# Kernel optimization log

Hardware: AMD Instinct MI355X
Metric: run time of the kernel (lower is better)

Reference implementation:

```python
import jax, jax.numpy as jnp
import numpy as np

NUM_ITEMS = 10000
EMBED_DIM = 64
USER_PERSPECTIVE_IMPORTANCE = 0.5
LEAKY_SLOPE = 0.2
BATCH = 32
MAX_HIST = 200


def setup_inputs() -> dict:
    key = jax.random.key(0)
    k_ids, k_len, k_items, k_user, k_w, k_b = jax.random.split(key, 6)
    batch_history_ids = jax.random.randint(k_ids, (BATCH, MAX_HIST), 0, NUM_ITEMS, dtype=jnp.int32)
    # lengths must be >= 1 to avoid all-masked softmax rows
    batch_history_lengths = jnp.maximum(
        jax.random.randint(k_len, (BATCH,), 0, MAX_HIST, dtype=jnp.int32), 1)
    items_embedding = jax.random.normal(k_items, (NUM_ITEMS, EMBED_DIM), dtype=jnp.float32)
    user_embedding = jax.random.normal(k_user, (1, EMBED_DIM), dtype=jnp.float32)
    fc_weight = jax.random.normal(k_w, (EMBED_DIM, EMBED_DIM), dtype=jnp.float32) * (1.0 / np.sqrt(EMBED_DIM))
    fc_bias = jax.random.normal(k_b, (EMBED_DIM,), dtype=jnp.float32) * 0.01
    return {
        'batch_history_ids': batch_history_ids,
        'batch_history_lengths': batch_history_lengths,
        'items_embedding': items_embedding,
        'user_embedding': user_embedding,
        'fc_weight': fc_weight,
        'fc_bias': fc_bias,
    }


def reference(batch_history_ids, batch_history_lengths, items_embedding, user_embedding, fc_weight, fc_bias):
    # valid[b, n] = n < length[b]
    valid = jnp.arange(MAX_HIST)[None, :] < batch_history_lengths[:, None]  # [B, N]

    hist_emb = items_embedding[batch_history_ids]  # [B, N, F] ragged gather (padded)

    # item-perspective attention: [B, I, N]
    item_att = jnp.einsum('if,bnf->bin', items_embedding, hist_emb)
    # original adds -inf mask then leaky_relu; leaky_relu(-inf) = -inf -> softmax weight 0
    item_att = jnp.where(valid[:, None, :], jax.nn.leaky_relu(item_att, LEAKY_SLOPE), -jnp.inf)
    item_scores = jax.nn.softmax(item_att, axis=-1)  # [B, I, N]

    # user-perspective attention: constant across the item-query axis (q=1, repeated over I),
    # so compute once as [B, N] and broadcast (same math as 'qif,bnf->bqin').
    user_att = jnp.einsum('f,bnf->bn', user_embedding[0], hist_emb)
    user_att = jnp.where(valid, jax.nn.leaky_relu(user_att, LEAKY_SLOPE), -jnp.inf)
    user_scores = jax.nn.softmax(user_att, axis=-1)  # [B, N]

    w = USER_PERSPECTIVE_IMPORTANCE
    attn = (1.0 - w) * item_scores + w * user_scores[:, None, :]  # [B, I, N]

    personalized = jnp.einsum('bin,bnf->bif', attn, hist_emb)  # [B, I, F]
    projected = personalized @ fc_weight.T + fc_bias  # [B, I, F]
    # final per-item score: dot with item embedding
    return jnp.einsum('bif,if->bi', projected, items_embedding)  # [B, I]
```

## Files before the change

### kernel.cpp

```cpp
#include <hip/hip_runtime.h>
#include <hip/hip_bf16.h>
#include <math.h>

#define NUM_ITEMS 10000
#define EMBED_DIM 64
#define MAX_HIST 200
#define NPAD 208
#define BATCH 32
#define LEAKY 0.2f
#define W_USER 0.5f
#define LOG2E 1.4426950408889634f
#define ECLAMP 110.0f

typedef short bf16x8 __attribute__((ext_vector_type(8)));
typedef float f32x4 __attribute__((ext_vector_type(4)));

__device__ __forceinline__ unsigned short f2bf(float f) {
    __hip_bfloat16 h = __float2bfloat16(f);
    return __builtin_bit_cast(unsigned short, h);
}

__device__ __forceinline__ float fexp2(float x) {
#if __has_builtin(__builtin_amdgcn_exp2f)
    return __builtin_amdgcn_exp2f(x);
#else
    return exp2f(x);
#endif
}

__global__ __launch_bounds__(256) void prep_kernel(const int* __restrict__ ids,
                                                   const int* __restrict__ lens,
                                                   const float* __restrict__ items,
                                                   const float* __restrict__ user,
                                                   const float* __restrict__ W,
                                                   const float* __restrict__ bias,
                                                   unsigned short* __restrict__ items_att_bf,
                                                   unsigned short* __restrict__ wti_bf,
                                                   float* __restrict__ bdot,
                                                   unsigned short* __restrict__ hist_bf,
                                                   unsigned short* __restrict__ uh_bf) {
    const int tid = threadIdx.x;
    __shared__ float shW[EMBED_DIM * EMBED_DIM];
    __shared__ float red[8];
    __shared__ float sh_usf[NPAD];
    __shared__ float sh_uh[4][EMBED_DIM];

    if (blockIdx.x < NUM_ITEMS / 4) {
        for (int idx = tid; idx < EMBED_DIM * EMBED_DIM; idx += 256) shW[idx] = W[idx];
        __syncthreads();

        const int i = blockIdx.x * 4 + (tid >> 6);
        const int g = tid & 63;
        const float* irow = items + i * EMBED_DIM;

        float acc = 0.f;
#pragma unroll
        for (int f = 0; f < EMBED_DIM; ++f) acc += irow[f] * shW[f * EMBED_DIM + g];

        wti_bf[i * EMBED_DIM + g] = f2bf(acc);
        items_att_bf[i * EMBED_DIM + g] = f2bf(irow[g] * LOG2E);

        float bv = bias[g] * irow[g];
#pragma unroll
        for (int o = 32; o > 0; o >>= 1) bv += __shfl_xor(bv, o, 64);
        if (g == 0) bdot[i] = bv;
    } else {
        const int b = blockIdx.x - NUM_ITEMS / 4;

        for (int idx = tid; idx < NPAD * 8; idx += 256) {
            const int n = idx >> 3, q = idx & 7;
            bf16x8 v = (bf16x8)0;
            if (n < MAX_HIST) {
                const int id = ids[b * MAX_HIST + n];
                const float4* p = (const float4*)(items + id * EMBED_DIM + q * 8);
                float4 v0 = p[0], v1 = p[1];
                v[0] = (short)f2bf(v0.x); v[1] = (short)f2bf(v0.y);
                v[2] = (short)f2bf(v0.z); v[3] = (short)f2bf(v0.w);
                v[4] = (short)f2bf(v1.x); v[5] = (short)f2bf(v1.y);
                v[6] = (short)f2bf(v1.z); v[7] = (short)f2bf(v1.w);
            }
            *(bf16x8*)(hist_bf + (size_t)(b * NPAD + n) * EMBED_DIM + q * 8) = v;
        }

        const int len = lens[b];
        float s = -INFINITY;
        if (tid < len) {
            const int id = ids[b * MAX_HIST + tid];
            const float* h = items + id * EMBED_DIM;
            float a0 = 0.f, a1 = 0.f;
#pragma unroll
            for (int f = 0; f < EMBED_DIM; f += 2) {
                a0 += user[f] * h[f];
                a1 += user[f + 1] * h[f + 1];
            }
            float a = a0 + a1;
            s = fmaxf(a, LEAKY * a);
        }
        float m = s;
#pragma unroll
        for (int o = 32; o > 0; o >>= 1) m = fmaxf(m, __shfl_xor(m, o, 64));
        if ((tid & 63) == 0) red[tid >> 6] = m;
        __syncthreads();
        m = fmaxf(fmaxf(red[0], red[1]), fmaxf(red[2], red[3]));

        float e = (tid < len) ? __expf(s - m) : 0.f;
        float t = e;
#pragma unroll
        for (int o = 32; o > 0; o >>= 1) t += __shfl_xor(t, o, 64);
        if ((tid & 63) == 0) red[4 + (tid >> 6)] = t;
        __syncthreads();
        const float sum = red[4] + red[5] + red[6] + red[7];

        if (tid < NPAD) sh_usf[tid] = (tid < len) ? (e / sum) : 0.f;
        __syncthreads();

        const int f = tid & 63;
        const int part = tid >> 6;
        float uhp = 0.f;
        for (int n = part; n < len; n += 4)
            uhp += sh_usf[n] * items[(size_t)ids[b * MAX_HIST + n] * EMBED_DIM + f];
        sh_uh[part][f] = uhp;
        __syncthreads();
        if (tid < EMBED_DIM)
            uh_bf[b * EMBED_DIM + tid] =
                f2bf(sh_uh[0][tid] + sh_uh[1][tid] + sh_uh[2][tid] + sh_uh[3][tid]);
    }
}

__global__ __launch_bounds__(256) void main_kernel(const unsigned short* __restrict__ items_att_bf,
                                                   const unsigned short* __restrict__ wti_bf,
                                                   const float* __restrict__ bdot,
                                                   const unsigned short* __restrict__ hist_bf,
                                                   const unsigned short* __restrict__ uh_bf,
                                                   const int* __restrict__ lens,
                                                   float* __restrict__ out) {
    const int b = blockIdx.y;
    const int tid = threadIdx.x;
    const int lane = tid & 63;
    const int w = tid >> 6;

    __shared__ __align__(16) unsigned short sh_hist[NPAD * EMBED_DIM];

    const int len = lens[b];
    const int ntiles = (len + 15) >> 4;

    const int c16 = lane & 15;
    const int g = lane >> 4;
    const int i0 = blockIdx.x * 128 + w * 32;
    const int iA = i0 + c16;
    const int iB = i0 + 16 + c16;

    bf16x8 itfA0 = *(const bf16x8*)(items_att_bf + (size_t)iA * 64 + g * 8);
    bf16x8 itfA1 = *(const bf16x8*)(items_att_bf + (size_t)iA * 64 + 32 + g * 8);
    bf16x8 wtfA0 = *(const bf16x8*)(wti_bf + (size_t)iA * 64 + g * 8);
    bf16x8 wtfA1 = *(const bf16x8*)(wti_bf + (size_t)iA * 64 + 32 + g * 8);
    bf16x8 itfB0 = *(const bf16x8*)(items_att_bf + (size_t)iB * 64 + g * 8);
    bf16x8 itfB1 = *(const bf16x8*)(items_att_bf + (size_t)iB * 64 + 32 + g * 8);
    bf16x8 wtfB0 = *(const bf16x8*)(wti_bf + (size_t)iB * 64 + g * 8);
    bf16x8 wtfB1 = *(const bf16x8*)(wti_bf + (size_t)iB * 64 + 32 + g * 8);
    bf16x8 u0 = *(const bf16x8*)(uh_bf + b * 64 + g * 8);
    bf16x8 u1 = *(const bf16x8*)(uh_bf + b * 64 + 32 + g * 8);

    const float4* src = (const float4*)(hist_bf + (size_t)b * NPAD * EMBED_DIM);
    const int nf4 = ntiles * 16 * 8;
    for (int c = tid; c < nf4; c += 256) {
        const int n = c >> 3, q = c & 7;
        float4 v = src[c];
        const int byte = (n * 128 + q * 16) ^ ((n & 7) << 4);
        *(float4*)((char*)sh_hist + byte) = v;
    }
    __syncthreads();

    if (i0 >= NUM_ITEMS) return;

    f32x4 sufA = (f32x4)0.f, sufB = (f32x4)0.f;
    sufA = __builtin_amdgcn_mfma_f32_16x16x32_bf16(u0, wtfA0, sufA, 0, 0, 0);
    sufA = __builtin_amdgcn_mfma_f32_16x16x32_bf16(u1, wtfA1, sufA, 0, 0, 0);
    sufB = __builtin_amdgcn_mfma_f32_16x16x32_bf16(u0, wtfB0, sufB, 0, 0, 0);
    sufB = __builtin_amdgcn_mfma_f32_16x16x32_bf16(u1, wtfB1, sufB, 0, 0, 0);
    const float SuA = sufA[0];
    const float SuB = sufB[0];

    float SeA = 0.f, ShA = 0.f, SeB = 0.f, ShB = 0.f;

    const char* hbase = (const char*)sh_hist;
#define LDA(T, X0, X1)                                                   \
    {                                                                    \
        const int n_ = (T) * 16 + c16;                                   \
        const int base_ = n_ * 128, sw_ = (n_ & 7) << 4;                 \
        X0 = *(const bf16x8*)(hbase + ((base_ + g * 16) ^ sw_));         \
        X1 = *(const bf16x8*)(hbase + ((base_ + 64 + g * 16) ^ sw_));    \
    }

#define EPI(S, H, Se, Sh, MASKED, NB)                                    \
    {                                                                    \
        float s0 = fminf(fmaxf(S[0], LEAKY * S[0]), ECLAMP);             \
        float s1 = fminf(fmaxf(S[1], LEAKY * S[1]), ECLAMP);             \
        float s2 = fminf(fmaxf(S[2], LEAKY * S[2]), ECLAMP);             \
        float s3 = fminf(fmaxf(S[3], LEAKY * S[3]), ECLAMP);             \
        if (MASKED) {                                                    \
            s0 = ((NB) + 0 < len) ? s0 : -INFINITY;                      \
            s1 = ((NB) + 1 < len) ? s1 : -INFINITY;                      \
            s2 = ((NB) + 2 < len) ? s2 : -INFINITY;                      \
            s3 = ((NB) + 3 < len) ? s3 : -INFINITY;                      \
        }                                                                \
        const float e0 = fexp2(s0), e1 = fexp2(s1);                      \
        const float e2 = fexp2(s2), e3 = fexp2(s3);                      \
        Se += (e0 + e1) + (e2 + e3);                                     \
        Sh = fmaf(e0, H[0], fmaf(e1, H[1], fmaf(e2, H[2], fmaf(e3, H[3], Sh)))); \
    }

#define MFMA8(A0, A1, SA, HA, SB, HB)                                     \
    SA = __builtin_amdgcn_mfma_f32_16x16x32_bf16(A0, itfA0, SA, 0, 0, 0); \
    SA = __builtin_amdgcn_mfma_f32_16x16x32_bf16(A1, itfA1, SA, 0, 0, 0); \
    SB = __builtin_amdgcn_mfma_f32_16x16x32_bf16(A0, itfB0, SB, 0, 0, 0); \
    SB = __builtin_amdgcn_mfma_f32_16x16x32_bf16(A1, itfB1, SB, 0, 0, 0); \
    HA = __builtin_amdgcn_mfma_f32_16x16x32_bf16(A0, wtfA0, HA, 0, 0, 0); \
    HA = __builtin_amdgcn_mfma_f32_16x16x32_bf16(A1, wtfA1, HA, 0, 0, 0); \
    HB = __builtin_amdgcn_mfma_f32_16x16x32_bf16(A0, wtfB0, HB, 0, 0, 0); \
    HB = __builtin_amdgcn_mfma_f32_16x16x32_bf16(A1, wtfB1, HB, 0, 0, 0);

    bf16x8 a0, a1;
    LDA(0, a0, a1)

    for (int t = 0; t < ntiles - 1; ++t) {
        f32x4 SA = (f32x4)0.f, HA = (f32x4)0.f, SB = (f32x4)0.f, HB = (f32x4)0.f;
        MFMA8(a0, a1, SA, HA, SB, HB)
        bf16x8 p0, p1;
        LDA(t + 1, p0, p1)
        const int nb = t * 16 + g * 4;
        (void)nb;
        EPI(SA, HA, SeA, ShA, 0, 0)
        EPI(SB, HB, SeB, ShB, 0, 0)
        a0 = p0; a1 = p1;
    }
    {
        f32x4 SA = (f32x4)0.f, HA = (f32x4)0.f, SB = (f32x4)0.f, HB = (f32x4)0.f;
        MFMA8(a0, a1, SA, HA, SB, HB)
        const int nb = (ntiles - 1) * 16 + g * 4;
        EPI(SA, HA, SeA, ShA, 1, nb)
        EPI(SB, HB, SeB, ShB, 1, nb)
    }
#undef MFMA8
#undef EPI
#undef LDA

    SeA += __shfl_xor(SeA, 16, 64); SeA += __shfl_xor(SeA, 32, 64);
    ShA += __shfl_xor(ShA, 16, 64); ShA += __shfl_xor(ShA, 32, 64);
    SeB += __shfl_xor(SeB, 16, 64); SeB += __shfl_xor(SeB, 32, 64);
    ShB += __shfl_xor(ShB, 16, 64); ShB += __shfl_xor(ShB, 32, 64);

    if (g == 0) {
        if (iA < NUM_ITEMS)
            out[(size_t)b * NUM_ITEMS + iA] =
                (1.0f - W_USER) * (ShA / SeA) + W_USER * SuA + bdot[iA];
        if (iB < NUM_ITEMS)
            out[(size_t)b * NUM_ITEMS + iB] =
                (1.0f - W_USER) * (ShB / SeB) + W_USER * SuB + bdot[iB];
    }
}

extern "C" void kernel_launch(void* const* d_in, const int* in_sizes, int n_in,
                              void* d_out, int out_size, void* d_ws, size_t ws_size,
                              hipStream_t stream) {
    const int* ids = (const int*)d_in[0];
    const int* lens = (const int*)d_in[1];
    const float* items = (const float*)d_in[2];
    const float* user = (const float*)d_in[3];
    const float* W = (const float*)d_in[4];
    const float* bias = (const float*)d_in[5];
    float* out = (float*)d_out;

    char* p = (char*)d_ws;
    unsigned short* items_att_bf = (unsigned short*)p; p += (size_t)NUM_ITEMS * EMBED_DIM * 2;
    unsigned short* wti_bf       = (unsigned short*)p; p += (size_t)NUM_ITEMS * EMBED_DIM * 2;
    float* bdot                  = (float*)p;          p += (size_t)NUM_ITEMS * 4;
    unsigned short* hist_bf      = (unsigned short*)p; p += (size_t)BATCH * NPAD * EMBED_DIM * 2;
    unsigned short* uh_bf        = (unsigned short*)p; p += (size_t)BATCH * EMBED_DIM * 2;

    prep_kernel<<<NUM_ITEMS / 4 + BATCH, 256, 0, stream>>>(ids, lens, items, user, W, bias,
                                                           items_att_bf, wti_bf, bdot,
                                                           hist_bf, uh_bf);

    dim3 grid((NUM_ITEMS + 127) / 128, BATCH);
    main_kernel<<<grid, 256, 0, stream>>>(items_att_bf, wti_bf, bdot, hist_bf, uh_bf, lens, out);
}
```

Measured before the change: 47.45 us.

## Amortize history staging over more items per block and shrink prep grid

The main kernel now covers 256 items per block instead of 128. Each wave processes four 16-item groups one after another, with the next group's item fragments prefetched, so the per-block LDS staging of the history tile is amortized over more items. The prep kernel uses 157 blocks, each handling 64 items in a loop, instead of 2500 tiny blocks. The user-weighted history sum now reads the bf16 history cached in LDS instead of re-gathering from global memory. The trade-offs are half as many main-kernel blocks (fewer waves in flight) and a serial dependency across item groups within each wave.

```diff
diff --git a/kernel.cpp b/kernel.cpp
--- a/kernel.cpp
+++ b/kernel.cpp
@@ -11,6 +11,7 @@
 #define W_USER 0.5f
 #define LOG2E 1.4426950408889634f
 #define ECLAMP 110.0f
+#define NWTI 157
 
 typedef short bf16x8 __attribute__((ext_vector_type(8)));
 typedef float f32x4 __attribute__((ext_vector_type(4)));
@@ -18,6 +19,10 @@
 __device__ __forceinline__ unsigned short f2bf(float f) {
     __hip_bfloat16 h = __float2bfloat16(f);
     return __builtin_bit_cast(unsigned short, h);
+}
+
+__device__ __forceinline__ float bf2f(unsigned short u) {
+    return __builtin_bit_cast(float, (unsigned int)u << 16);
 }
 
 __device__ __forceinline__ float fexp2(float x) {
@@ -40,32 +45,40 @@
                                                    unsigned short* __restrict__ hist_bf,
                                                    unsigned short* __restrict__ uh_bf) {
     const int tid = threadIdx.x;
-    __shared__ float shW[EMBED_DIM * EMBED_DIM];
+    __shared__ __align__(16) char sbuf[NPAD * EMBED_DIM * 2];
     __shared__ float red[8];
     __shared__ float sh_usf[NPAD];
     __shared__ float sh_uh[4][EMBED_DIM];
 
-    if (blockIdx.x < NUM_ITEMS / 4) {
+    if (blockIdx.x < NWTI) {
+        float* shW = (float*)sbuf;
         for (int idx = tid; idx < EMBED_DIM * EMBED_DIM; idx += 256) shW[idx] = W[idx];
         __syncthreads();
 
-        const int i = blockIdx.x * 4 + (tid >> 6);
         const int g = tid & 63;
-        const float* irow = items + i * EMBED_DIM;
-
-        float acc = 0.f;
-#pragma unroll
-        for (int f = 0; f < EMBED_DIM; ++f) acc += irow[f] * shW[f * EMBED_DIM + g];
-
-        wti_bf[i * EMBED_DIM + g] = f2bf(acc);
-        items_att_bf[i * EMBED_DIM + g] = f2bf(irow[g] * LOG2E);
-
-        float bv = bias[g] * irow[g];
-#pragma unroll
-        for (int o = 32; o > 0; o >>= 1) bv += __shfl_xor(bv, o, 64);
-        if (g == 0) bdot[i] = bv;
+        const int isub = tid >> 6;
+        const int base = blockIdx.x * 64 + isub * 16;
+
+        for (int k = 0; k < 16; ++k) {
+            const int i = base + k;
+            if (i >= NUM_ITEMS) break;
+            const float* irow = items + (size_t)i * EMBED_DIM;
+
+            float acc = 0.f;
+#pragma unroll
+            for (int f = 0; f < EMBED_DIM; ++f) acc += irow[f] * shW[f * EMBED_DIM + g];
+
+            wti_bf[i * EMBED_DIM + g] = f2bf(acc);
+            items_att_bf[i * EMBED_DIM + g] = f2bf(irow[g] * LOG2E);
+
+            float bv = bias[g] * irow[g];
+#pragma unroll
+            for (int o = 32; o > 0; o >>= 1) bv += __shfl_xor(bv, o, 64);
+            if (g == 0) bdot[i] = bv;
+        }
     } else {
-        const int b = blockIdx.x - NUM_ITEMS / 4;
+        const int b = blockIdx.x - NWTI;
+        unsigned short* sh_h = (unsigned short*)sbuf;
 
         for (int idx = tid; idx < NPAD * 8; idx += 256) {
             const int n = idx >> 3, q = idx & 7;
@@ -80,6 +93,7 @@
                 v[6] = (short)f2bf(v1.z); v[7] = (short)f2bf(v1.w);
             }
             *(bf16x8*)(hist_bf + (size_t)(b * NPAD + n) * EMBED_DIM + q * 8) = v;
+            *(bf16x8*)(sh_h + (size_t)n * EMBED_DIM + q * 8) = v;
         }
 
         const int len = lens[b];
@@ -118,7 +132,7 @@
         const int part = tid >> 6;
         float uhp = 0.f;
         for (int n = part; n < len; n += 4)
-            uhp += sh_usf[n] * items[(size_t)ids[b * MAX_HIST + n] * EMBED_DIM + f];
+            uhp += sh_usf[n] * bf2f(sh_h[n * EMBED_DIM + f]);
         sh_uh[part][f] = uhp;
         __syncthreads();
         if (tid < EMBED_DIM)
@@ -146,18 +160,7 @@
 
     const int c16 = lane & 15;
     const int g = lane >> 4;
-    const int i0 = blockIdx.x * 128 + w * 32;
-    const int iA = i0 + c16;
-    const int iB = i0 + 16 + c16;
-
-    bf16x8 itfA0 = *(const bf16x8*)(items_att_bf + (size_t)iA * 64 + g * 8);
-    bf16x8 itfA1 = *(const bf16x8*)(items_att_bf + (size_t)iA * 64 + 32 + g * 8);
-    bf16x8 wtfA0 = *(const bf16x8*)(wti_bf + (size_t)iA * 64 + g * 8);
-    bf16x8 wtfA1 = *(const bf16x8*)(wti_bf + (size_t)iA * 64 + 32 + g * 8);
-    bf16x8 itfB0 = *(const bf16x8*)(items_att_bf + (size_t)iB * 64 + g * 8);
-    bf16x8 itfB1 = *(const bf16x8*)(items_att_bf + (size_t)iB * 64 + 32 + g * 8);
-    bf16x8 wtfB0 = *(const bf16x8*)(wti_bf + (size_t)iB * 64 + g * 8);
-    bf16x8 wtfB1 = *(const bf16x8*)(wti_bf + (size_t)iB * 64 + 32 + g * 8);
+
     bf16x8 u0 = *(const bf16x8*)(uh_bf + b * 64 + g * 8);
     bf16x8 u1 = *(const bf16x8*)(uh_bf + b * 64 + 32 + g * 8);
 
@@ -171,19 +174,8 @@
     }
     __syncthreads();
 
-    if (i0 >= NUM_ITEMS) return;
-
-    f32x4 sufA = (f32x4)0.f, sufB = (f32x4)0.f;
-    sufA = __builtin_amdgcn_mfma_f32_16x16x32_bf16(u0, wtfA0, sufA, 0, 0, 0);
-    sufA = __builtin_amdgcn_mfma_f32_16x16x32_bf16(u1, wtfA1, sufA, 0, 0, 0);
-    sufB = __builtin_amdgcn_mfma_f32_16x16x32_bf16(u0, wtfB0, sufB, 0, 0, 0);
-    sufB = __builtin_amdgcn_mfma_f32_16x16x32_bf16(u1, wtfB1, sufB, 0, 0, 0);
-    const float SuA = sufA[0];
-    const float SuB = sufB[0];
-
-    float SeA = 0.f, ShA = 0.f, SeB = 0.f, ShB = 0.f;
-
     const char* hbase = (const char*)sh_hist;
+
 #define LDA(T, X0, X1)                                                   \
     {                                                                    \
         const int n_ = (T) * 16 + c16;                                   \
@@ -210,54 +202,71 @@
         Sh = fmaf(e0, H[0], fmaf(e1, H[1], fmaf(e2, H[2], fmaf(e3, H[3], Sh)))); \
     }
 
-#define MFMA8(A0, A1, SA, HA, SB, HB)                                     \
-    SA = __builtin_amdgcn_mfma_f32_16x16x32_bf16(A0, itfA0, SA, 0, 0, 0); \
-    SA = __builtin_amdgcn_mfma_f32_16x16x32_bf16(A1, itfA1, SA, 0, 0, 0); \
-    SB = __builtin_amdgcn_mfma_f32_16x16x32_bf16(A0, itfB0, SB, 0, 0, 0); \
-    SB = __builtin_amdgcn_mfma_f32_16x16x32_bf16(A1, itfB1, SB, 0, 0, 0); \
-    HA = __builtin_amdgcn_mfma_f32_16x16x32_bf16(A0, wtfA0, HA, 0, 0, 0); \
-    HA = __builtin_amdgcn_mfma_f32_16x16x32_bf16(A1, wtfA1, HA, 0, 0, 0); \
-    HB = __builtin_amdgcn_mfma_f32_16x16x32_bf16(A0, wtfB0, HB, 0, 0, 0); \
-    HB = __builtin_amdgcn_mfma_f32_16x16x32_bf16(A1, wtfB1, HB, 0, 0, 0);
-
-    bf16x8 a0, a1;
-    LDA(0, a0, a1)
-
-    for (int t = 0; t < ntiles - 1; ++t) {
-        f32x4 SA = (f32x4)0.f, HA = (f32x4)0.f, SB = (f32x4)0.f, HB = (f32x4)0.f;
-        MFMA8(a0, a1, SA, HA, SB, HB)
-        bf16x8 p0, p1;
-        LDA(t + 1, p0, p1)
-        const int nb = t * 16 + g * 4;
-        (void)nb;
-        EPI(SA, HA, SeA, ShA, 0, 0)
-        EPI(SB, HB, SeB, ShB, 0, 0)
-        a0 = p0; a1 = p1;
-    }
-    {
-        f32x4 SA = (f32x4)0.f, HA = (f32x4)0.f, SB = (f32x4)0.f, HB = (f32x4)0.f;
-        MFMA8(a0, a1, SA, HA, SB, HB)
-        const int nb = (ntiles - 1) * 16 + g * 4;
-        EPI(SA, HA, SeA, ShA, 1, nb)
-        EPI(SB, HB, SeB, ShB, 1, nb)
-    }
-#undef MFMA8
+    const int wbase = blockIdx.x * 256 + w * 16;
+
+    int ild = min(wbase + c16, NUM_ITEMS - 1);
+    bf16x8 itc0 = *(const bf16x8*)(items_att_bf + (size_t)ild * 64 + g * 8);
+    bf16x8 itc1 = *(const bf16x8*)(items_att_bf + (size_t)ild * 64 + 32 + g * 8);
+    bf16x8 wtc0 = *(const bf16x8*)(wti_bf + (size_t)ild * 64 + g * 8);
+    bf16x8 wtc1 = *(const bf16x8*)(wti_bf + (size_t)ild * 64 + 32 + g * 8);
+
+#pragma unroll
+    for (int it = 0; it < 4; ++it) {
+        const int gstart = wbase + it * 64;
+        if (gstart >= NUM_ITEMS) break;
+
+        bf16x8 nt0, nt1, nw0, nw1;
+        if (it < 3) {
+            const int inx = min(wbase + (it + 1) * 64 + c16, NUM_ITEMS - 1);
+            nt0 = *(const bf16x8*)(items_att_bf + (size_t)inx * 64 + g * 8);
+            nt1 = *(const bf16x8*)(items_att_bf + (size_t)inx * 64 + 32 + g * 8);
+            nw0 = *(const bf16x8*)(wti_bf + (size_t)inx * 64 + g * 8);
+            nw1 = *(const bf16x8*)(wti_bf + (size_t)inx * 64 + 32 + g * 8);
+        }
+
+        f32x4 suf = (f32x4)0.f;
+        suf = __builtin_amdgcn_mfma_f32_16x16x32_bf16(u0, wtc0, suf, 0, 0, 0);
+        suf = __builtin_amdgcn_mfma_f32_16x16x32_bf16(u1, wtc1, suf, 0, 0, 0);
+        const float Su = suf[0];
+
+        float Se = 0.f, Sh = 0.f;
+        bf16x8 a0, a1;
+        LDA(0, a0, a1)
+
+        for (int t = 0; t < ntiles - 1; ++t) {
+            f32x4 S = (f32x4)0.f, H = (f32x4)0.f;
+            S = __builtin_amdgcn_mfma_f32_16x16x32_bf16(a0, itc0, S, 0, 0, 0);
+            S = __builtin_amdgcn_mfma_f32_16x16x32_bf16(a1, itc1, S, 0, 0, 0);
+            H = __builtin_amdgcn_mfma_f32_16x16x32_bf16(a0, wtc0, H, 0, 0, 0);
+            H = __builtin_amdgcn_mfma_f32_16x16x32_bf16(a1, wtc1, H, 0, 0, 0);
+            bf16x8 p0, p1;
+            LDA(t + 1, p0, p1)
+            EPI(S, H, Se, Sh, 0, 0)
+            a0 = p0; a1 = p1;
+        }
+        {
+            f32x4 S = (f32x4)0.f, H = (f32x4)0.f;
+            S = __builtin_amdgcn_mfma_f32_16x16x32_bf16(a0, itc0, S, 0, 0, 0);
+            S = __builtin_amdgcn_mfma_f32_16x16x32_bf16(a1, itc1, S, 0, 0, 0);
+            H = __builtin_amdgcn_mfma_f32_16x16x32_bf16(a0, wtc0, H, 0, 0, 0);
+            H = __builtin_amdgcn_mfma_f32_16x16x32_bf16(a1, wtc1, H, 0, 0, 0);
+            const int nb = (ntiles - 1) * 16 + g * 4;
+            EPI(S, H, Se, Sh, 1, nb)
+        }
+
+        Se += __shfl_xor(Se, 16, 64); Se += __shfl_xor(Se, 32, 64);
+        Sh += __shfl_xor(Sh, 16, 64); Sh += __shfl_xor(Sh, 32, 64);
+
+        if (g == 0) {
+            const int i = gstart + c16;
+            out[(size_t)b * NUM_ITEMS + i] =
+                (1.0f - W_USER) * (Sh / Se) + W_USER * Su + bdot[i];
+        }
+
+        if (it < 3) { itc0 = nt0; itc1 = nt1; wtc0 = nw0; wtc1 = nw1; }
+    }
 #undef EPI
 #undef LDA
-
-    SeA += __shfl_xor(SeA, 16, 64); SeA += __shfl_xor(SeA, 32, 64);
-    ShA += __shfl_xor(ShA, 16, 64); ShA += __shfl_xor(ShA, 32, 64);
-    SeB += __shfl_xor(SeB, 16, 64); SeB += __shfl_xor(SeB, 32, 64);
-    ShB += __shfl_xor(ShB, 16, 64); ShB += __shfl_xor(ShB, 32, 64);
-
-    if (g == 0) {
-        if (iA < NUM_ITEMS)
-            out[(size_t)b * NUM_ITEMS + iA] =
-                (1.0f - W_USER) * (ShA / SeA) + W_USER * SuA + bdot[iA];
-        if (iB < NUM_ITEMS)
-            out[(size_t)b * NUM_ITEMS + iB] =
-                (1.0f - W_USER) * (ShB / SeB) + W_USER * SuB + bdot[iB];
-    }
 }
 
 extern "C" void kernel_launch(void* const* d_in, const int* in_sizes, int n_in,
@@ -278,10 +287,10 @@
     unsigned short* hist_bf      = (unsigned short*)p; p += (size_t)BATCH * NPAD * EMBED_DIM * 2;
     unsigned short* uh_bf        = (unsigned short*)p; p += (size_t)BATCH * EMBED_DIM * 2;
 
-    prep_kernel<<<NUM_ITEMS / 4 + BATCH, 256, 0, stream>>>(ids, lens, items, user, W, bias,
-                                                           items_att_bf, wti_bf, bdot,
-                                                           hist_bf, uh_bf);
-
-    dim3 grid((NUM_ITEMS + 127) / 128, BATCH);
+    prep_kernel<<<NWTI + BATCH, 256, 0, stream>>>(ids, lens, items, user, W, bias,
+                                                  items_att_bf, wti_bf, bdot,
+                                                  hist_bf, uh_bf);
+
+    dim3 grid((NUM_ITEMS + 255) / 256, BATCH);
     main_kernel<<<grid, 256, 0, stream>>>(items_att_bf, wti_bf, bdot, hist_bf, uh_bf, lens, out);
 }
```

Result: faster. 44.58 us (-6.0%).
